# Kernel optimization log

Hardware: AMD Instinct MI355X
Metric: run time of the kernel (lower is better)

The kernel has to match this reference:

```python
import jax, jax.numpy as jnp
import numpy as np

N_NODES = 50000
N_EDGES = 800000  # random edges, guaranteed no self loops; self loops appended explicitly
D_FEAT = 128
N_LAYERS = 4


def setup_inputs() -> dict:
    key = jax.random.key(0)
    k1, k2, k3, k4 = jax.random.split(key, 4)
    src = jax.random.randint(k1, (N_EDGES,), 0, N_NODES)
    # offset in [1, N-1] guarantees dst != src (module removes self loops anyway)
    off = jax.random.randint(k2, (N_EDGES,), 1, N_NODES)
    dst = (src + off) % N_NODES
    # add_self_loop: append i->i for every node (module does this every layer;
    # with drop_edge p=0 the per-layer graph is identical, so build once)
    loops = jnp.arange(N_NODES)
    src = jnp.concatenate([src, loops])
    dst = jnp.concatenate([dst, loops])
    in_feat = jax.random.normal(k3, (N_NODES, D_FEAT), jnp.float32)
    Ws = jax.random.normal(k4, (N_LAYERS, D_FEAT, D_FEAT), jnp.float32) / np.sqrt(D_FEAT)
    bs = jnp.zeros((N_LAYERS, D_FEAT), jnp.float32)
    return {"in_feat": in_feat, "Ws": Ws, "bs": bs, "src": src, "dst": dst}


def reference(in_feat, Ws, bs, src, dst):
    # JKNet: L x [dropout(p=0) -> GraphConv(norm='both') -> LeakyReLU], then JK max.
    N = in_feat.shape[0]
    ones = jnp.ones(src.shape[0], in_feat.dtype)
    deg_out = jax.ops.segment_sum(ones, src, num_segments=N)  # out-degree (src norm)
    deg_in = jax.ops.segment_sum(ones, dst, num_segments=N)   # in-degree  (dst norm)
    norm_src = jnp.maximum(deg_out, 1.0) ** -0.5
    norm_dst = jnp.maximum(deg_in, 1.0) ** -0.5

    feat_list = [in_feat]
    x = in_feat
    for l in range(Ws.shape[0]):
        h = x * norm_src[:, None]
        agg = jax.ops.segment_sum(h[src], dst, num_segments=N)  # [N, d] sparse aggregation
        h = agg * norm_dst[:, None]
        h = h @ Ws[l] + bs[l]
        x = jax.nn.leaky_relu(h, negative_slope=0.01)  # nn.LeakyReLU default
        feat_list.append(x)

    # Jumping-knowledge max pooling over layer outputs (torch.max values)
    return jnp.max(jnp.stack(feat_list, axis=-1), axis=-1)
```

## Files before the change

kernel.cpp:

```cpp
#include <hip/hip_runtime.h>
#include <cstdint>

#define D 128
#define MAXDEG 64

typedef __attribute__((ext_vector_type(8))) short bf16x8;
typedef __attribute__((ext_vector_type(4))) float f32x4;

__device__ __forceinline__ unsigned short f2b(float f) {
  unsigned u = __float_as_uint(f);
  return (unsigned short)((u + 0x7fffu + ((u >> 16) & 1u)) >> 16);
}
__device__ __forceinline__ float blo(unsigned u) { return __uint_as_float(u << 16); }
__device__ __forceinline__ float bhi(unsigned u) { return __uint_as_float(u & 0xffff0000u); }

__global__ __launch_bounds__(256) void init_kernel(int* __restrict__ cursor,
    int* __restrict__ dego, int N) {
  int i = blockIdx.x * 256 + threadIdx.x;
  if (i < N) {
    cursor[i] = i * MAXDEG;
    dego[i] = 0;
  }
}

__global__ __launch_bounds__(256) void fill_deg(const int* __restrict__ src,
    const int* __restrict__ dst, int* __restrict__ cursor,
    int* __restrict__ esrc, int* __restrict__ dego, int Er) {
  int e = blockIdx.x * 256 + threadIdx.x;
  if (e < Er) {
    int s = src[e];
    int d = dst[e];
    int slot = atomicAdd(cursor + d, 1);
    esrc[slot] = s;
    atomicAdd(dego + s, 1);
  }
}

__global__ __launch_bounds__(256) void norm_kernel(const int* __restrict__ dego,
    const int* __restrict__ cursor, float* __restrict__ ns,
    float* __restrict__ nd, int N) {
  int i = blockIdx.x * 256 + threadIdx.x;
  if (i < N) {
    ns[i] = rsqrtf((float)(dego[i] + 1));
    nd[i] = rsqrtf((float)(cursor[i] - i * MAXDEG + 1));
  }
}

template<bool INF32>
__global__ __launch_bounds__(256, 4) void gemm_mfma(const float* __restrict__ xf,
    const unsigned short* __restrict__ xb, const float* __restrict__ nsrc,
    const float* __restrict__ W, unsigned short* __restrict__ zout, int N) {
  __shared__ unsigned short Wt[D * D];
  for (int i = threadIdx.x; i < D * D; i += 256) {
    int k = i >> 7;
    int c = i & 127;
    Wt[(c * D + k) ^ ((c & 7) << 3)] = f2b(W[i]);
  }
  __syncthreads();

  int wave = threadIdx.x >> 6;
  int lane = threadIdx.x & 63;
  int r16 = lane & 15;
  int kgrp = lane >> 4;
  int rw = blockIdx.x * 64 + wave * 16;

  f32x4 acc[8] = {};
  int gr = rw + r16;
  if (gr >= N) gr = N - 1;

  #pragma unroll
  for (int ks = 0; ks < 4; ++ks) {
    int k0 = ks * 32 + kgrp * 8;
    bf16x8 a;
    if (INF32) {
      const float4* p = (const float4*)(xf + (size_t)gr * D + k0);
      float4 lo = p[0], hi = p[1];
      a[0] = (short)f2b(lo.x); a[1] = (short)f2b(lo.y);
      a[2] = (short)f2b(lo.z); a[3] = (short)f2b(lo.w);
      a[4] = (short)f2b(hi.x); a[5] = (short)f2b(hi.y);
      a[6] = (short)f2b(hi.z); a[7] = (short)f2b(hi.w);
    } else {
      a = *(const bf16x8*)(xb + (size_t)gr * D + k0);
    }
    #pragma unroll
    for (int ct = 0; ct < 8; ++ct) {
      int c = ct * 16 + r16;
      bf16x8 b = *(const bf16x8*)(Wt + ((c * D + k0) ^ ((c & 7) << 3)));
      acc[ct] = __builtin_amdgcn_mfma_f32_16x16x32_bf16(a, b, acc[ct], 0, 0, 0);
    }
  }

  #pragma unroll
  for (int q = 0; q < 4; ++q) {
    int row = rw + kgrp * 4 + q;
    if (row < N) {
      float ns = nsrc[row];
      #pragma unroll
      for (int ct = 0; ct < 8; ++ct) {
        zout[(size_t)row * D + ct * 16 + r16] = f2b(acc[ct][q] * ns);
      }
    }
  }
}

struct Acc8 {
  float a0, a1, a2, a3, a4, a5, a6, a7;
  __device__ __forceinline__ void zero() {
    a0 = a1 = a2 = a3 = a4 = a5 = a6 = a7 = 0.f;
  }
  __device__ __forceinline__ void add(uint4 v) {
    a0 += blo(v.x); a1 += bhi(v.x); a2 += blo(v.y); a3 += bhi(v.y);
    a4 += blo(v.z); a5 += bhi(v.z); a6 += blo(v.w); a7 += bhi(v.w);
  }
};

template<bool INJ32, bool OUTJ32>
__global__ __launch_bounds__(256, 8) void gather_kernel(
    const unsigned short* __restrict__ z, const int* __restrict__ row_end,
    const int* __restrict__ esrc, const float* __restrict__ ndst,
    const float* __restrict__ bias, const float* __restrict__ jkinf,
    const unsigned short* __restrict__ jkinb, unsigned short* __restrict__ xb_out,
    float* __restrict__ jkoutf, unsigned short* __restrict__ jkoutb,
    int N, int write_x) {
  int t = blockIdx.x * 256 + threadIdx.x;
  int row = t >> 4;
  if (row >= N) return;
  int cg = t & 15;
  const uint4* zp = (const uint4*)z;

  int b = row * MAXDEG;
  int e = row_end[row];
  Acc8 A;
  A.zero();
  A.add(zp[(size_t)row * 16 + cg]);

  int j = b;
  for (; j + 3 < e; j += 4) {
    int4 s = *(const int4*)(esrc + j);
    uint4 v0 = zp[(size_t)s.x * 16 + cg];
    uint4 v1 = zp[(size_t)s.y * 16 + cg];
    uint4 v2 = zp[(size_t)s.z * 16 + cg];
    uint4 v3 = zp[(size_t)s.w * 16 + cg];
    A.add(v0); A.add(v1); A.add(v2); A.add(v3);
  }
  for (; j < e; ++j) {
    A.add(zp[(size_t)esrc[j] * 16 + cg]);
  }

  float nd = ndst[row];
  float4 bv0 = ((const float4*)bias)[cg * 2];
  float4 bv1 = ((const float4*)bias)[cg * 2 + 1];
  float4 o0, o1;
  o0.x = nd * A.a0 + bv0.x; o0.y = nd * A.a1 + bv0.y;
  o0.z = nd * A.a2 + bv0.z; o0.w = nd * A.a3 + bv0.w;
  o1.x = nd * A.a4 + bv1.x; o1.y = nd * A.a5 + bv1.y;
  o1.z = nd * A.a6 + bv1.z; o1.w = nd * A.a7 + bv1.w;
  o0.x = o0.x > 0.f ? o0.x : 0.01f * o0.x;
  o0.y = o0.y > 0.f ? o0.y : 0.01f * o0.y;
  o0.z = o0.z > 0.f ? o0.z : 0.01f * o0.z;
  o0.w = o0.w > 0.f ? o0.w : 0.01f * o0.w;
  o1.x = o1.x > 0.f ? o1.x : 0.01f * o1.x;
  o1.y = o1.y > 0.f ? o1.y : 0.01f * o1.y;
  o1.z = o1.z > 0.f ? o1.z : 0.01f * o1.z;
  o1.w = o1.w > 0.f ? o1.w : 0.01f * o1.w;

  if (write_x) {
    uint4 px;
    px.x = (unsigned)f2b(o0.x) | ((unsigned)f2b(o0.y) << 16);
    px.y = (unsigned)f2b(o0.z) | ((unsigned)f2b(o0.w) << 16);
    px.z = (unsigned)f2b(o1.x) | ((unsigned)f2b(o1.y) << 16);
    px.w = (unsigned)f2b(o1.z) | ((unsigned)f2b(o1.w) << 16);
    ((uint4*)xb_out)[(size_t)row * 16 + cg] = px;
  }

  float4 m0, m1;
  if (INJ32) {
    m0 = ((const float4*)jkinf)[(size_t)row * 32 + cg * 2];
    m1 = ((const float4*)jkinf)[(size_t)row * 32 + cg * 2 + 1];
  } else {
    uint4 mj = ((const uint4*)jkinb)[(size_t)row * 16 + cg];
    m0.x = blo(mj.x); m0.y = bhi(mj.x); m0.z = blo(mj.y); m0.w = bhi(mj.y);
    m1.x = blo(mj.z); m1.y = bhi(mj.z); m1.z = blo(mj.w); m1.w = bhi(mj.w);
  }
  m0.x = fmaxf(m0.x, o0.x); m0.y = fmaxf(m0.y, o0.y);
  m0.z = fmaxf(m0.z, o0.z); m0.w = fmaxf(m0.w, o0.w);
  m1.x = fmaxf(m1.x, o1.x); m1.y = fmaxf(m1.y, o1.y);
  m1.z = fmaxf(m1.z, o1.z); m1.w = fmaxf(m1.w, o1.w);
  if (OUTJ32) {
    ((float4*)jkoutf)[(size_t)row * 32 + cg * 2] = m0;
    ((float4*)jkoutf)[(size_t)row * 32 + cg * 2 + 1] = m1;
  } else {
    uint4 pm;
    pm.x = (unsigned)f2b(m0.x) | ((unsigned)f2b(m0.y) << 16);
    pm.y = (unsigned)f2b(m0.z) | ((unsigned)f2b(m0.w) << 16);
    pm.z = (unsigned)f2b(m1.x) | ((unsigned)f2b(m1.y) << 16);
    pm.w = (unsigned)f2b(m1.z) | ((unsigned)f2b(m1.w) << 16);
    ((uint4*)jkoutb)[(size_t)row * 16 + cg] = pm;
  }
}

extern "C" void kernel_launch(void* const* d_in, const int* in_sizes, int n_in,
                              void* d_out, int out_size, void* d_ws, size_t ws_size,
                              hipStream_t stream) {
  const float* in_feat = (const float*)d_in[0];
  const float* Ws = (const float*)d_in[1];
  const float* bs = (const float*)d_in[2];
  const int* src = (const int*)d_in[3];
  const int* dst = (const int*)d_in[4];
  int N = in_sizes[0] / D;
  int L = in_sizes[2] / D;
  int E = in_sizes[3];
  float* out = (float*)d_out;

  int Er = E - N;
  if (Er < 0) Er = E;

  int nb = (N + 255) / 256;

  char* p = (char*)d_ws;
  int* dego   = (int*)p;   p += (size_t)N * 4;
  int* cursor = (int*)p;   p += (size_t)N * 4;
  int* esrc   = (int*)p;   p += (size_t)N * MAXDEG * 4;
  float* nsrc = (float*)p; p += (size_t)N * 4;
  float* ndst = (float*)p; p += (size_t)N * 4;
  unsigned short* z   = (unsigned short*)p; p += (size_t)N * D * 2;
  unsigned short* xb  = (unsigned short*)p; p += (size_t)N * D * 2;
  unsigned short* jkb = (unsigned short*)p;

  init_kernel<<<nb, 256, 0, stream>>>(cursor, dego, N);
  fill_deg<<<(Er + 255) / 256, 256, 0, stream>>>(src, dst, cursor, esrc, dego, Er);
  norm_kernel<<<nb, 256, 0, stream>>>(dego, cursor, nsrc, ndst, N);

  int mb = (N + 63) / 64;
  int gb = (int)(((long long)N * 16 + 255) / 256);
  for (int l = 0; l < L; ++l) {
    if (l == 0) {
      gemm_mfma<true><<<mb, 256, 0, stream>>>(in_feat, nullptr, nsrc, Ws, z, N);
    } else {
      gemm_mfma<false><<<mb, 256, 0, stream>>>(nullptr, xb, nsrc,
                                               Ws + (size_t)l * D * D, z, N);
    }
    const float* bias = bs + (size_t)l * D;
    int wx = (l + 1 < L) ? 1 : 0;
    if (l == 0 && L == 1) {
      gather_kernel<true, true><<<gb, 256, 0, stream>>>(z, cursor, esrc,
          ndst, bias, in_feat, nullptr, xb, out, nullptr, N, wx);
    } else if (l == 0) {
      gather_kernel<true, false><<<gb, 256, 0, stream>>>(z, cursor, esrc,
          ndst, bias, in_feat, nullptr, xb, nullptr, jkb, N, wx);
    } else if (l == L - 1) {
      gather_kernel<false, true><<<gb, 256, 0, stream>>>(z, cursor, esrc,
          ndst, bias, nullptr, jkb, xb, out, nullptr, N, wx);
    } else {
      gather_kernel<false, false><<<gb, 256, 0, stream>>>(z, cursor, esrc,
          ndst, bias, nullptr, jkb, xb, nullptr, jkb, N, wx);
    }
  }
}
```

Measured before the change: 286.4 us.

## Precompute bf16 swizzled weights once and double rows per GEMM block

Adds a prep kernel that converts all layer weights to swizzled bf16 once, so each GEMM block copies them into LDS with vector loads instead of converting fp32 per block. Each block now processes 128 rows (two 16-row tiles per wave), reusing each LDS weight fragment for two MFMAs and halving the number of blocks that stage W. This costs more accumulator registers and one extra small kernel launch, and leaves fewer blocks to spread across CUs.

```diff
diff --git a/kernel.cpp b/kernel.cpp
--- a/kernel.cpp
+++ b/kernel.cpp
@@ -46,15 +46,29 @@
   }
 }
 
+__global__ __launch_bounds__(256) void prep_w(const float* __restrict__ Ws,
+    unsigned short* __restrict__ Wt, int total) {
+  int i = blockIdx.x * 256 + threadIdx.x;
+  if (i < total) {
+    int l = i >> 14;
+    int rem = i & 16383;
+    int k = rem >> 7;
+    int c = rem & 127;
+    Wt[(l << 14) + (((c << 7) + k) ^ ((c & 7) << 3))] = f2b(Ws[i]);
+  }
+}
+
 template<bool INF32>
 __global__ __launch_bounds__(256, 4) void gemm_mfma(const float* __restrict__ xf,
     const unsigned short* __restrict__ xb, const float* __restrict__ nsrc,
-    const float* __restrict__ W, unsigned short* __restrict__ zout, int N) {
-  __shared__ unsigned short Wt[D * D];
-  for (int i = threadIdx.x; i < D * D; i += 256) {
-    int k = i >> 7;
-    int c = i & 127;
-    Wt[(c * D + k) ^ ((c & 7) << 3)] = f2b(W[i]);
+    const unsigned short* __restrict__ Wt, unsigned short* __restrict__ zout,
+    int N) {
+  __shared__ unsigned short Wl[D * D];
+  {
+    const uint4* s4 = (const uint4*)Wt;
+    uint4* d4 = (uint4*)Wl;
+    #pragma unroll
+    for (int i = 0; i < 8; ++i) d4[threadIdx.x + i * 256] = s4[threadIdx.x + i * 256];
   }
   __syncthreads();
 
@@ -62,43 +76,59 @@
   int lane = threadIdx.x & 63;
   int r16 = lane & 15;
   int kgrp = lane >> 4;
-  int rw = blockIdx.x * 64 + wave * 16;
-
-  f32x4 acc[8] = {};
-  int gr = rw + r16;
-  if (gr >= N) gr = N - 1;
+  int rw0 = blockIdx.x * 128 + wave * 16;
+  int rw1 = rw0 + 64;
+
+  f32x4 acc0[8] = {};
+  f32x4 acc1[8] = {};
+  int gr0 = rw0 + r16; if (gr0 >= N) gr0 = N - 1;
+  int gr1 = rw1 + r16; if (gr1 >= N) gr1 = N - 1;
 
   #pragma unroll
   for (int ks = 0; ks < 4; ++ks) {
     int k0 = ks * 32 + kgrp * 8;
-    bf16x8 a;
+    bf16x8 a0, a1;
     if (INF32) {
-      const float4* p = (const float4*)(xf + (size_t)gr * D + k0);
-      float4 lo = p[0], hi = p[1];
-      a[0] = (short)f2b(lo.x); a[1] = (short)f2b(lo.y);
-      a[2] = (short)f2b(lo.z); a[3] = (short)f2b(lo.w);
-      a[4] = (short)f2b(hi.x); a[5] = (short)f2b(hi.y);
-      a[6] = (short)f2b(hi.z); a[7] = (short)f2b(hi.w);
+      const float4* p0 = (const float4*)(xf + (size_t)gr0 * D + k0);
+      float4 lo = p0[0], hi = p0[1];
+      a0[0] = (short)f2b(lo.x); a0[1] = (short)f2b(lo.y);
+      a0[2] = (short)f2b(lo.z); a0[3] = (short)f2b(lo.w);
+      a0[4] = (short)f2b(hi.x); a0[5] = (short)f2b(hi.y);
+      a0[6] = (short)f2b(hi.z); a0[7] = (short)f2b(hi.w);
+      const float4* p1 = (const float4*)(xf + (size_t)gr1 * D + k0);
+      lo = p1[0]; hi = p1[1];
+      a1[0] = (short)f2b(lo.x); a1[1] = (short)f2b(lo.y);
+      a1[2] = (short)f2b(lo.z); a1[3] = (short)f2b(lo.w);
+      a1[4] = (short)f2b(hi.x); a1[5] = (short)f2b(hi.y);
+      a1[6] = (short)f2b(hi.z); a1[7] = (short)f2b(hi.w);
     } else {
-      a = *(const bf16x8*)(xb + (size_t)gr * D + k0);
+      a0 = *(const bf16x8*)(xb + (size_t)gr0 * D + k0);
+      a1 = *(const bf16x8*)(xb + (size_t)gr1 * D + k0);
     }
     #pragma unroll
     for (int ct = 0; ct < 8; ++ct) {
       int c = ct * 16 + r16;
-      bf16x8 b = *(const bf16x8*)(Wt + ((c * D + k0) ^ ((c & 7) << 3)));
-      acc[ct] = __builtin_amdgcn_mfma_f32_16x16x32_bf16(a, b, acc[ct], 0, 0, 0);
+      bf16x8 b = *(const bf16x8*)(Wl + (((c << 7) + k0) ^ ((c & 7) << 3)));
+      acc0[ct] = __builtin_amdgcn_mfma_f32_16x16x32_bf16(a0, b, acc0[ct], 0, 0, 0);
+      acc1[ct] = __builtin_amdgcn_mfma_f32_16x16x32_bf16(a1, b, acc1[ct], 0, 0, 0);
     }
   }
 
   #pragma unroll
   for (int q = 0; q < 4; ++q) {
-    int row = rw + kgrp * 4 + q;
-    if (row < N) {
-      float ns = nsrc[row];
+    int row0 = rw0 + kgrp * 4 + q;
+    if (row0 < N) {
+      float ns = nsrc[row0];
       #pragma unroll
-      for (int ct = 0; ct < 8; ++ct) {
-        zout[(size_t)row * D + ct * 16 + r16] = f2b(acc[ct][q] * ns);
-      }
+      for (int ct = 0; ct < 8; ++ct)
+        zout[(size_t)row0 * D + ct * 16 + r16] = f2b(acc0[ct][q] * ns);
+    }
+    int row1 = rw1 + kgrp * 4 + q;
+    if (row1 < N) {
+      float ns = nsrc[row1];
+      #pragma unroll
+      for (int ct = 0; ct < 8; ++ct)
+        zout[(size_t)row1 * D + ct * 16 + r16] = f2b(acc1[ct][q] * ns);
     }
   }
 }
@@ -223,6 +253,7 @@
   int* esrc   = (int*)p;   p += (size_t)N * MAXDEG * 4;
   float* nsrc = (float*)p; p += (size_t)N * 4;
   float* ndst = (float*)p; p += (size_t)N * 4;
+  unsigned short* wt  = (unsigned short*)p; p += (size_t)L * D * D * 2;
   unsigned short* z   = (unsigned short*)p; p += (size_t)N * D * 2;
   unsigned short* xb  = (unsigned short*)p; p += (size_t)N * D * 2;
   unsigned short* jkb = (unsigned short*)p;
@@ -230,15 +261,17 @@
   init_kernel<<<nb, 256, 0, stream>>>(cursor, dego, N);
   fill_deg<<<(Er + 255) / 256, 256, 0, stream>>>(src, dst, cursor, esrc, dego, Er);
   norm_kernel<<<nb, 256, 0, stream>>>(dego, cursor, nsrc, ndst, N);
-
-  int mb = (N + 63) / 64;
+  int wtot = L * D * D;
+  prep_w<<<(wtot + 255) / 256, 256, 0, stream>>>(Ws, wt, wtot);
+
+  int mb = (N + 127) / 128;
   int gb = (int)(((long long)N * 16 + 255) / 256);
   for (int l = 0; l < L; ++l) {
+    const unsigned short* wl = wt + (size_t)l * D * D;
     if (l == 0) {
-      gemm_mfma<true><<<mb, 256, 0, stream>>>(in_feat, nullptr, nsrc, Ws, z, N);
+      gemm_mfma<true><<<mb, 256, 0, stream>>>(in_feat, nullptr, nsrc, wl, z, N);
     } else {
-      gemm_mfma<false><<<mb, 256, 0, stream>>>(nullptr, xb, nsrc,
-                                               Ws + (size_t)l * D * D, z, N);
+      gemm_mfma<false><<<mb, 256, 0, stream>>>(nullptr, xb, nsrc, wl, z, N);
     }
     const float* bias = bs + (size_t)l * D;
     int wx = (l + 1 < L) ? 1 : 0;
```

Result: faster. 276.0 us (median of 2 runs) (-3.6%).
